# Kernel optimization log

Measured on AMD Instinct MI355X. Metric: run time of the kernel, lower is better.

## Reference

```python
import jax, jax.numpy as jnp
import numpy as np

NEG_BIG = -9e15
ALPHA = 0.2  # LeakyReLU negative slope
B, N, F_IN, F_OUT = 8, 2048, 128, 128


def setup_inputs() -> dict:
    key = jax.random.key(0)
    k1, k2, k3, k4 = jax.random.split(key, 4)
    inp = jax.random.normal(k1, (B, N, F_IN), dtype=jnp.float32)
    adj = jax.random.randint(k2, (B, N, N), 0, 2, dtype=jnp.int32)
    W = 0.02 * jax.random.normal(k3, (F_OUT, F_IN), dtype=jnp.float32)  # nn.Linear weight [out,in]
    a = 0.02 * jax.random.normal(k4, (1, 2 * F_OUT), dtype=jnp.float32)  # attention vector [1, 2F]
    return {"input": inp, "adj": adj, "W": W, "a": a}


def reference(input, adj, W, a):
    # h = input @ W^T : [B, N, F_OUT]
    h = jnp.einsum("bnf,of->bno", input, W)
    f_out = h.shape[-1]
    # Decompose a . [h_i || h_j] = (h_i . a1) + (h_j . a2) -- same math as the
    # explicit repeat_interleave/repeat/cat, without the O(N^2 * 2F) tensor.
    a1 = a[0, :f_out]
    a2 = a[0, f_out:]
    s1 = h @ a1  # [B, N] score for source node i
    s2 = h @ a2  # [B, N] score for target node j
    e = jax.nn.leaky_relu(s1[:, :, None] + s2[:, None, :], negative_slope=ALPHA)  # [B,N,N]
    masked = jnp.where(adj > 0, e, NEG_BIG)
    attention = jax.nn.softmax(masked, axis=-1)
    # dropout p=0.0 (eval) -> identity
    h_prime = jnp.einsum("bnm,bmo->bno", attention, h)
    return h_prime
```

## Files before the change

### kernel.cpp

```cpp
#include <hip/hip_runtime.h>
#include <stdint.h>


#define B_ 8
#define N_ 2048
#define FD 128
#define ALPHA_ 0.2f
#define TJ 64
#define NCHL 16
#define CHUNK_U4 1024

typedef __attribute__((ext_vector_type(8))) short short8;
typedef __attribute__((ext_vector_type(4))) float f32x4;

#define HC64(o, jc) ((o) * 8 + ((jc) ^ ((o) & 7)))

__device__ __forceinline__ float bf2f(unsigned short u) {
    union { uint32_t i; float f; } v; v.i = ((uint32_t)u) << 16; return v.f;
}
__device__ __forceinline__ unsigned short f2bf(float f) {
    union { float f; uint32_t i; } v; v.f = f;
    uint32_t x = v.i;
    uint32_t r = (x + 0x7fffu + ((x >> 16) & 1u)) >> 16;
    return (unsigned short)r;
}

__device__ __forceinline__ void gl2lds16(const uint4* g, uint4* l) {
    __builtin_amdgcn_global_load_lds(
        (const __attribute__((address_space(1))) uint32_t*)g,
        (__attribute__((address_space(3))) uint32_t*)l, 16, 0, 0);
}

__global__ __launch_bounds__(256, 4) void gat_h(
    const float* __restrict__ x,
    const float* __restrict__ W,
    const float* __restrict__ a,
    unsigned short* __restrict__ hT,
    float* __restrict__ s1o, float* __restrict__ s2o)
{
    __shared__ __align__(16) uint4 xs[32][32];
    __shared__ float s1c[2][32], s2c[2][32];

    const int bid = blockIdx.x;
    const int tid = threadIdx.x;
    const int w = tid >> 6;
    const int lane = tid & 63;
    const int oh = w >> 1;
    const int rh = w & 1;
    const int m = lane & 15;
    const int quad = lane >> 4;

#pragma unroll
    for (int it = 0; it < 4; it++) {
        int idx = it * 256 + tid;
        int row = idx >> 5, c = idx & 31;
        uint4 v = *(const uint4*)(x + (size_t)bid * 4096 + (size_t)idx * 4);
        xs[row][c ^ row] = v;
    }
    __syncthreads();

    f32x4 acc[4];
#pragma unroll
    for (int ot = 0; ot < 4; ot++) acc[ot] = (f32x4){0.f, 0.f, 0.f, 0.f};

    const int xrow = rh * 16 + m;
#pragma unroll
    for (int ks = 0; ks < 4; ks++) {
        const int c0 = ks * 8 + quad * 2;
        union { uint4 u[2]; float f[8]; } xv;
        xv.u[0] = xs[xrow][c0 ^ xrow];
        xv.u[1] = xs[xrow][(c0 + 1) ^ xrow];
        union { unsigned short us[8]; short8 v; } ahi, alo;
#pragma unroll
        for (int jj = 0; jj < 8; jj++) {
            unsigned short hi = f2bf(xv.f[jj]);
            ahi.us[jj] = hi;
            alo.us[jj] = f2bf(xv.f[jj] - bf2f(hi));
        }
#pragma unroll
        for (int ot = 0; ot < 4; ot++) {
            const int o = (oh * 4 + ot) * 16 + m;
            const float* wp = W + (size_t)o * FD + ks * 32 + quad * 8;
            float4 w0 = *(const float4*)wp;
            float4 w1 = *(const float4*)(wp + 4);
            union { unsigned short us[8]; short8 v; } bw;
            bw.us[0] = f2bf(w0.x); bw.us[1] = f2bf(w0.y);
            bw.us[2] = f2bf(w0.z); bw.us[3] = f2bf(w0.w);
            bw.us[4] = f2bf(w1.x); bw.us[5] = f2bf(w1.y);
            bw.us[6] = f2bf(w1.z); bw.us[7] = f2bf(w1.w);
            acc[ot] = __builtin_amdgcn_mfma_f32_16x16x32_bf16(ahi.v, bw.v, acc[ot], 0, 0, 0);
            acc[ot] = __builtin_amdgcn_mfma_f32_16x16x32_bf16(alo.v, bw.v, acc[ot], 0, 0, 0);
        }
    }

    const int gr = bid * 32 + rh * 16 + quad * 4;
    const int bb = gr >> 11;
    const int jb = gr & (N_ - 1);
    const int kc = jb >> 6;
    const int jcl = (jb & 63) >> 3;
    const int off = jb & 7;
    unsigned short* hTb = hT + (size_t)bb * FD * N_ + (size_t)kc * (CHUNK_U4 * 8);
    float s1p[4] = {0.f, 0.f, 0.f, 0.f};
    float s2p[4] = {0.f, 0.f, 0.f, 0.f};
#pragma unroll
    for (int ot = 0; ot < 4; ot++) {
        const int o = (oh * 4 + ot) * 16 + m;
        uint2 pk;
        pk.x = (uint32_t)f2bf(acc[ot][0]) | ((uint32_t)f2bf(acc[ot][1]) << 16);
        pk.y = (uint32_t)f2bf(acc[ot][2]) | ((uint32_t)f2bf(acc[ot][3]) << 16);
        *(uint2*)(hTb + (size_t)HC64(o, jcl) * 8 + off) = pk;
        float a1v = a[o], a2v = a[FD + o];
#pragma unroll
        for (int r = 0; r < 4; r++) {
            s1p[r] += acc[ot][r] * a1v;
            s2p[r] += acc[ot][r] * a2v;
        }
    }
#pragma unroll
    for (int offx = 8; offx >= 1; offx >>= 1) {
#pragma unroll
        for (int r = 0; r < 4; r++) {
            s1p[r] += __shfl_xor(s1p[r], offx);
            s2p[r] += __shfl_xor(s2p[r], offx);
        }
    }
    if (m == 0) {
#pragma unroll
        for (int r = 0; r < 4; r++) {
            s1c[oh][rh * 16 + quad * 4 + r] = s1p[r];
            s2c[oh][rh * 16 + quad * 4 + r] = s2p[r];
        }
    }
    __syncthreads();
    if (tid < 32) {
        s1o[bid * 32 + tid] = s1c[0][tid] + s1c[1][tid];
        s2o[bid * 32 + tid] = s2c[0][tid] + s2c[1][tid];
    }
}

__global__ __launch_bounds__(256, 2) void gat_attn(
    const int* __restrict__ adj,
    const unsigned short* __restrict__ hT,
    const float* __restrict__ s1,
    const float* __restrict__ s2,
    float* __restrict__ out)
{
    __shared__ __align__(16) uint4 hbuf[2][2][CHUNK_U4];

    const int bid = blockIdx.x;
    const int b = bid & 7;
    const int i0 = (bid >> 3) * 32;
    const int tid = threadIdx.x;
    const int lane = tid & 63;
    const int w = tid >> 6;
    const int jh = w >> 1;
    const int rh = w & 1;
    const int m = lane & 15;
    const int quad = lane >> 4;

    const int irow = i0 + rh * 16 + m;
    const float s1v = s1[b * N_ + irow];
    const int* adjrow = adj + ((size_t)(b * N_ + irow)) * N_ + jh * 1024;
    const uint4* hTc = (const uint4*)(hT + (size_t)b * FD * N_)
                       + (size_t)jh * NCHL * CHUNK_U4;
    const float* s2b = s2 + b * N_ + jh * 1024;

#pragma unroll
    for (int it = 0; it < 8; it++)
        gl2lds16(&hTc[it * 128 + rh * 64 + lane], &hbuf[jh][0][it * 128 + rh * 64]);
    int4 acur[4];
    float4 scur[4];
#pragma unroll
    for (int ks = 0; ks < 2; ks++) {
        acur[2 * ks]     = *(const int4*)(adjrow + ks * 32 + quad * 8);
        acur[2 * ks + 1] = *(const int4*)(adjrow + ks * 32 + quad * 8 + 4);
        scur[2 * ks]     = *(const float4*)(s2b + ks * 32 + quad * 8);
        scur[2 * ks + 1] = *(const float4*)(s2b + ks * 32 + quad * 8 + 4);
    }
    __syncthreads();

    f32x4 acc[8];
#pragma unroll
    for (int ot = 0; ot < 8; ot++) acc[ot] = (f32x4){0.f, 0.f, 0.f, 0.f};
    float rs_loc = 0.f;

    for (int k = 0; k < NCHL; k++) {
        const int buf = k & 1;
        const bool more = (k + 1 < NCHL);
        int4 anext[4];
        float4 snext[4];
        if (more) {
#pragma unroll
            for (int it = 0; it < 8; it++)
                gl2lds16(&hTc[(size_t)(k + 1) * CHUNK_U4 + it * 128 + rh * 64 + lane],
                         &hbuf[jh][buf ^ 1][it * 128 + rh * 64]);
            const int j1 = (k + 1) * TJ;
#pragma unroll
            for (int ks = 0; ks < 2; ks++) {
                anext[2 * ks]     = *(const int4*)(adjrow + j1 + ks * 32 + quad * 8);
                anext[2 * ks + 1] = *(const int4*)(adjrow + j1 + ks * 32 + quad * 8 + 4);
                snext[2 * ks]     = *(const float4*)(s2b + j1 + ks * 32 + quad * 8);
                snext[2 * ks + 1] = *(const float4*)(s2b + j1 + ks * 32 + quad * 8 + 4);
            }
        }

#pragma unroll
        for (int ks = 0; ks < 2; ks++) {
            float4 sa = scur[2 * ks], sb = scur[2 * ks + 1];
            float sarr[8] = {sa.x, sa.y, sa.z, sa.w, sb.x, sb.y, sb.z, sb.w};
            int4 A0 = acur[2 * ks], A1 = acur[2 * ks + 1];
            int aarr[8] = {A0.x, A0.y, A0.z, A0.w, A1.x, A1.y, A1.z, A1.w};
            union { unsigned short us[8]; short8 v; } af;
#pragma unroll
            for (int jj = 0; jj < 8; jj++) {
                float e = s1v + sarr[jj];
                e = (e > 0.f) ? e : (ALPHA_ * e);
                float p = (aarr[jj] > 0) ? __expf(e) : 0.f;
                rs_loc += p;
                af.us[jj] = f2bf(p);
            }
            const int jc = ks * 4 + quad;
#pragma unroll
            for (int ot = 0; ot < 8; ot++) {
                const int o = ot * 16 + m;
                union { uint4 u; short8 v; } bf;
                bf.u = *(const uint4*)&hbuf[jh][buf][HC64(o, jc)];
                acc[ot] = __builtin_amdgcn_mfma_f32_16x16x32_bf16(af.v, bf.v, acc[ot], 0, 0, 0);
            }
        }

        __syncthreads();
        if (more) {
#pragma unroll
            for (int q = 0; q < 4; q++) { acur[q] = anext[q]; scur[q] = snext[q]; }
        }
    }

    float* xch = (float*)&hbuf[0][0][0];
    rs_loc += __shfl_xor(rs_loc, 16);
    rs_loc += __shfl_xor(rs_loc, 32);
    if (jh == 1) {
#pragma unroll
        for (int ot = 0; ot < 8; ot++)
#pragma unroll
            for (int r = 0; r < 4; r++)
                xch[rh * 2048 + (quad * 4 + r) * 128 + ot * 16 + m] = acc[ot][r];
        if (quad == 0) xch[4096 + rh * 16 + m] = rs_loc;
    }
    __syncthreads();
    if (jh == 0) {
        float rinv[4];
#pragma unroll
        for (int r = 0; r < 4; r++) {
            const int p = quad * 4 + r;
            rinv[r] = 1.0f / (__shfl(rs_loc, p) + xch[4096 + rh * 16 + p]);
        }
        float* outp = out + (size_t)(b * N_ + i0 + rh * 16) * FD;
#pragma unroll
        for (int ot = 0; ot < 8; ot++) {
            const int col = ot * 16 + m;
#pragma unroll
            for (int r = 0; r < 4; r++) {
                float v = acc[ot][r] + xch[rh * 2048 + (quad * 4 + r) * 128 + col];
                outp[(size_t)(quad * 4 + r) * FD + col] = v * rinv[r];
            }
        }
    }
}

extern "C" void kernel_launch(void* const* d_in, const int* in_sizes, int n_in,
                              void* d_out, int out_size, void* d_ws, size_t ws_size,
                              hipStream_t stream) {
    const void* xv = d_in[0];
    const void* adjv = d_in[1];
    const void* Wv = d_in[2];
    const void* av = d_in[3];
    for (int i = 0; i < n_in; i++) {
        switch (in_sizes[i]) {
            case 2097152:  xv = d_in[i]; break;
            case 33554432: adjv = d_in[i]; break;
            case 16384:    Wv = d_in[i]; break;
            case 256:      av = d_in[i]; break;
            default: break;
        }
    }
    const float* x = (const float*)xv;
    const int* adj = (const int*)adjv;
    const float* W = (const float*)Wv;
    const float* a = (const float*)av;
    float* out = (float*)d_out;

    char* p = (char*)d_ws;
    unsigned short* hT = (unsigned short*)p;  p += (size_t)B_ * FD * N_ * 2;
    float* s1 = (float*)p;                    p += (size_t)B_ * N_ * 4;
    float* s2 = (float*)p;

    gat_h<<<512, 256, 0, stream>>>(x, W, a, hT, s1, s2);
    gat_attn<<<512, 256, 0, stream>>>(adj, hT, s1, s2, out);
}
```

Measured before the change: 222.7 us.

## Read hT directly from global memory and split j range across four waves

The attention kernel no longer stages hT chunks into LDS with async loads, double buffering and per-chunk barriers. Each wave instead reads its B operand straight from global/L2 and handles a quarter of the j range for 16 rows. The grid is doubled to 1024 blocks and partial results are reduced through LDS at the end. This removes the barrier and LDS staging costs, but hT is now re-read from cache by every wave with 16-byte gathered loads, and the adjacency prefetching is lost.

```diff
diff --git a/kernel.cpp b/kernel.cpp
--- a/kernel.cpp
+++ b/kernel.cpp
@@ -6,8 +6,6 @@
 #define N_ 2048
 #define FD 128
 #define ALPHA_ 0.2f
-#define TJ 64
-#define NCHL 16
 #define CHUNK_U4 1024
 
 typedef __attribute__((ext_vector_type(8))) short short8;
@@ -23,12 +21,6 @@
     uint32_t x = v.i;
     uint32_t r = (x + 0x7fffu + ((x >> 16) & 1u)) >> 16;
     return (unsigned short)r;
-}
-
-__device__ __forceinline__ void gl2lds16(const uint4* g, uint4* l) {
-    __builtin_amdgcn_global_load_lds(
-        (const __attribute__((address_space(1))) uint32_t*)g,
-        (__attribute__((address_space(3))) uint32_t*)l, 16, 0, 0);
 }
 
 __global__ __launch_bounds__(256, 4) void gat_h(
@@ -138,77 +130,55 @@
     }
 }
 
-__global__ __launch_bounds__(256, 2) void gat_attn(
+__global__ __launch_bounds__(256, 3) void gat_attn(
     const int* __restrict__ adj,
     const unsigned short* __restrict__ hT,
     const float* __restrict__ s1,
     const float* __restrict__ s2,
     float* __restrict__ out)
 {
-    __shared__ __align__(16) uint4 hbuf[2][2][CHUNK_U4];
+    __shared__ float part[3][16][128];
+    __shared__ float prs[3][16];
 
     const int bid = blockIdx.x;
     const int b = bid & 7;
-    const int i0 = (bid >> 3) * 32;
+    const int i0 = (bid >> 3) * 16;
     const int tid = threadIdx.x;
     const int lane = tid & 63;
     const int w = tid >> 6;
-    const int jh = w >> 1;
-    const int rh = w & 1;
     const int m = lane & 15;
     const int quad = lane >> 4;
 
-    const int irow = i0 + rh * 16 + m;
+    const int irow = i0 + m;
     const float s1v = s1[b * N_ + irow];
-    const int* adjrow = adj + ((size_t)(b * N_ + irow)) * N_ + jh * 1024;
-    const uint4* hTc = (const uint4*)(hT + (size_t)b * FD * N_)
-                       + (size_t)jh * NCHL * CHUNK_U4;
-    const float* s2b = s2 + b * N_ + jh * 1024;
-
-#pragma unroll
-    for (int it = 0; it < 8; it++)
-        gl2lds16(&hTc[it * 128 + rh * 64 + lane], &hbuf[jh][0][it * 128 + rh * 64]);
-    int4 acur[4];
-    float4 scur[4];
-#pragma unroll
-    for (int ks = 0; ks < 2; ks++) {
-        acur[2 * ks]     = *(const int4*)(adjrow + ks * 32 + quad * 8);
-        acur[2 * ks + 1] = *(const int4*)(adjrow + ks * 32 + quad * 8 + 4);
-        scur[2 * ks]     = *(const float4*)(s2b + ks * 32 + quad * 8);
-        scur[2 * ks + 1] = *(const float4*)(s2b + ks * 32 + quad * 8 + 4);
-    }
-    __syncthreads();
+    const int* adjrow = adj + ((size_t)(b * N_ + irow)) * N_ + w * 512;
+    const uint4* hTq = (const uint4*)(hT + (size_t)b * FD * N_)
+                       + (size_t)w * 8 * CHUNK_U4;
+    const float* s2b = s2 + b * N_ + w * 512;
 
     f32x4 acc[8];
 #pragma unroll
     for (int ot = 0; ot < 8; ot++) acc[ot] = (f32x4){0.f, 0.f, 0.f, 0.f};
     float rs_loc = 0.f;
 
-    for (int k = 0; k < NCHL; k++) {
-        const int buf = k & 1;
-        const bool more = (k + 1 < NCHL);
-        int4 anext[4];
-        float4 snext[4];
-        if (more) {
-#pragma unroll
-            for (int it = 0; it < 8; it++)
-                gl2lds16(&hTc[(size_t)(k + 1) * CHUNK_U4 + it * 128 + rh * 64 + lane],
-                         &hbuf[jh][buf ^ 1][it * 128 + rh * 64]);
-            const int j1 = (k + 1) * TJ;
-#pragma unroll
-            for (int ks = 0; ks < 2; ks++) {
-                anext[2 * ks]     = *(const int4*)(adjrow + j1 + ks * 32 + quad * 8);
-                anext[2 * ks + 1] = *(const int4*)(adjrow + j1 + ks * 32 + quad * 8 + 4);
-                snext[2 * ks]     = *(const float4*)(s2b + j1 + ks * 32 + quad * 8);
-                snext[2 * ks + 1] = *(const float4*)(s2b + j1 + ks * 32 + quad * 8 + 4);
-            }
-        }
-
+#pragma unroll 2
+    for (int k = 0; k < 8; k++) {
+        const int j0 = k * 64;
+        int4 A[4];
+        float4 S[4];
 #pragma unroll
         for (int ks = 0; ks < 2; ks++) {
-            float4 sa = scur[2 * ks], sb = scur[2 * ks + 1];
+            A[2 * ks]     = *(const int4*)(adjrow + j0 + ks * 32 + quad * 8);
+            A[2 * ks + 1] = *(const int4*)(adjrow + j0 + ks * 32 + quad * 8 + 4);
+            S[2 * ks]     = *(const float4*)(s2b + j0 + ks * 32 + quad * 8);
+            S[2 * ks + 1] = *(const float4*)(s2b + j0 + ks * 32 + quad * 8 + 4);
+        }
+        const uint4* hc = hTq + (size_t)k * CHUNK_U4;
+#pragma unroll
+        for (int ks = 0; ks < 2; ks++) {
+            float4 sa = S[2 * ks], sb = S[2 * ks + 1];
             float sarr[8] = {sa.x, sa.y, sa.z, sa.w, sb.x, sb.y, sb.z, sb.w};
-            int4 A0 = acur[2 * ks], A1 = acur[2 * ks + 1];
+            int4 A0 = A[2 * ks], A1 = A[2 * ks + 1];
             int aarr[8] = {A0.x, A0.y, A0.z, A0.w, A1.x, A1.y, A1.z, A1.w};
             union { unsigned short us[8]; short8 v; } af;
 #pragma unroll
@@ -224,45 +194,40 @@
             for (int ot = 0; ot < 8; ot++) {
                 const int o = ot * 16 + m;
                 union { uint4 u; short8 v; } bf;
-                bf.u = *(const uint4*)&hbuf[jh][buf][HC64(o, jc)];
+                bf.u = hc[HC64(o, jc)];
                 acc[ot] = __builtin_amdgcn_mfma_f32_16x16x32_bf16(af.v, bf.v, acc[ot], 0, 0, 0);
             }
         }
-
-        __syncthreads();
-        if (more) {
-#pragma unroll
-            for (int q = 0; q < 4; q++) { acur[q] = anext[q]; scur[q] = snext[q]; }
-        }
-    }
-
-    float* xch = (float*)&hbuf[0][0][0];
+    }
+
     rs_loc += __shfl_xor(rs_loc, 16);
     rs_loc += __shfl_xor(rs_loc, 32);
-    if (jh == 1) {
+    if (w > 0) {
 #pragma unroll
         for (int ot = 0; ot < 8; ot++)
 #pragma unroll
             for (int r = 0; r < 4; r++)
-                xch[rh * 2048 + (quad * 4 + r) * 128 + ot * 16 + m] = acc[ot][r];
-        if (quad == 0) xch[4096 + rh * 16 + m] = rs_loc;
+                part[w - 1][quad * 4 + r][ot * 16 + m] = acc[ot][r];
+        if (quad == 0) prs[w - 1][m] = rs_loc;
     }
     __syncthreads();
-    if (jh == 0) {
+    if (w == 0) {
         float rinv[4];
 #pragma unroll
         for (int r = 0; r < 4; r++) {
             const int p = quad * 4 + r;
-            rinv[r] = 1.0f / (__shfl(rs_loc, p) + xch[4096 + rh * 16 + p]);
-        }
-        float* outp = out + (size_t)(b * N_ + i0 + rh * 16) * FD;
+            rinv[r] = 1.0f / (__shfl(rs_loc, p) + prs[0][p] + prs[1][p] + prs[2][p]);
+        }
+        float* outp = out + (size_t)(b * N_ + i0) * FD;
 #pragma unroll
         for (int ot = 0; ot < 8; ot++) {
             const int col = ot * 16 + m;
 #pragma unroll
             for (int r = 0; r < 4; r++) {
-                float v = acc[ot][r] + xch[rh * 2048 + (quad * 4 + r) * 128 + col];
-                outp[(size_t)(quad * 4 + r) * FD + col] = v * rinv[r];
+                const int row = quad * 4 + r;
+                float v = acc[ot][r] + part[0][row][col] + part[1][row][col]
+                                     + part[2][row][col];
+                outp[(size_t)row * FD + col] = v * rinv[r];
             }
         }
     }
@@ -296,5 +261,5 @@
     float* s2 = (float*)p;
 
     gat_h<<<512, 256, 0, stream>>>(x, W, a, hT, s1, s2);
-    gat_attn<<<512, 256, 0, stream>>>(adj, hT, s1, s2, out);
-}
+    gat_attn<<<1024, 256, 0, stream>>>(adj, hT, s1, s2, out);
+}
```

Measured after the change: 265.6 us. +19.3%, slower.
